# Optimization experiments

Hardware: AMD Instinct MI355X
Metric: run time of the kernel (lower is better)

Reference implementation:

```python
import jax, jax.numpy as jnp
import numpy as np

B, N, NPOINT, NSAMPLE = 8, 8192, 2048, 32
RADIUS = 0.4
C_IN = 64
MLP = [64, 64, 128]
EPS = 1e-5
BIG = 1e10


def setup_inputs() -> dict:
    key = jax.random.key(0)
    ks = jax.random.split(key, 2 + 4 * len(MLP))
    inp = {
        'xyz': jax.random.normal(ks[0], (B, N, 3), jnp.float32),
        'features': jax.random.normal(ks[1], (B, C_IN, N), jnp.float32),
    }
    last_c = C_IN + 3
    j = 2
    for i, out_c in enumerate(MLP):
        inp[f'w{i}'] = jax.random.normal(ks[j], (out_c, last_c), jnp.float32) * (1.0 / np.sqrt(last_c)); j += 1
        inp[f'b{i}'] = jax.random.normal(ks[j], (out_c,), jnp.float32) * 0.01; j += 1
        inp[f'g{i}'] = 1.0 + 0.01 * jax.random.normal(ks[j], (out_c,), jnp.float32); j += 1
        inp[f'bt{i}'] = 0.01 * jax.random.normal(ks[j], (out_c,), jnp.float32); j += 1
        last_c = out_c
    return inp


def fps(xyz, m):
    # Farthest point sampling; deterministic start at index 0 (torch uses randint).
    b, n, _ = xyz.shape

    def step(carry, _):
        dist, far = carry
        centroid = jnp.take_along_axis(xyz, far[:, None, None], axis=1)  # [B,1,3]
        d = jnp.sum((xyz - centroid) ** 2, axis=-1)                      # [B,N]
        dist = jnp.minimum(dist, d)
        new_far = jnp.argmax(dist, axis=1)
        return (dist, new_far), far

    init = (jnp.full((b, n), BIG, xyz.dtype), jnp.zeros((b,), jnp.int32))
    _, idxs = jax.lax.scan(step, init, None, length=m)
    return jnp.transpose(idxs)  # [B,m]


def ball_query(xyz, centroids, radius, k):
    # Euclidean cdist via the (a-b)^2 = a^2 + b^2 - 2ab expansion.
    x2 = jnp.sum(xyz * xyz, axis=-1)            # [B,N]
    c2 = jnp.sum(centroids * centroids, axis=-1)  # [B,M]
    d2 = c2[:, :, None] + x2[:, None, :] - 2.0 * jnp.einsum('bmd,bnd->bmn', centroids, xyz)
    d = jnp.sqrt(jnp.maximum(d2, 0.0))           # [B,M,N]
    dm = jnp.where(d <= radius, d, BIG)
    _, idx = jax.lax.top_k(-dm, k)               # k smallest distances
    return idx                                   # [B,M,K]


def gather_points(x, idx):
    # x: [B,N,C], idx: [B,M,K] -> [B,M,K,C]
    b = x.shape[0]
    return x[jnp.arange(b)[:, None, None], idx]


def reference(xyz, features, w0, b0, g0, bt0, w1, b1, g1, bt1, w2, b2, g2, bt2):
    idx = fps(xyz, NPOINT)                                   # [B,M]
    new_xyz = jnp.take_along_axis(xyz, idx[:, :, None], axis=1)  # [B,M,3]
    knn_idx = ball_query(xyz, new_xyz, RADIUS, NSAMPLE)      # [B,M,K]
    grouped_xyz = gather_points(xyz, knn_idx)                # [B,M,K,3]
    grouped_xyz_norm = grouped_xyz - new_xyz[:, :, None, :]
    grouped_feat = gather_points(jnp.transpose(features, (0, 2, 1)), knn_idx)  # [B,M,K,C]
    feat = jnp.concatenate([grouped_xyz_norm, grouped_feat], axis=-1)          # [B,M,K,C+3]

    for w, b, g, bt in ((w0, b0, g0, bt0), (w1, b1, g1, bt1), (w2, b2, g2, bt2)):
        feat = jnp.einsum('bmkc,oc->bmko', feat, w) + b      # 1x1 conv
        mu = jnp.mean(feat, axis=(0, 1, 2))                  # BN, training-mode batch stats
        var = jnp.mean((feat - mu) ** 2, axis=(0, 1, 2))
        feat = (feat - mu) * jax.lax.rsqrt(var + EPS) * g + bt
        feat = jax.nn.relu(feat)

    new_feat = jnp.max(feat, axis=2)                         # max over neighbors -> [B,M,C_out]
    return new_xyz, jnp.transpose(new_feat, (0, 2, 1))       # [B,M,3], [B,C_out,M]
```

## Files before the change

kernel.cpp:

```cpp
#include <hip/hip_runtime.h>
#include <hip/hip_bf16.h>
#include <stdint.h>

typedef unsigned short u16;
typedef unsigned int   u32;
typedef unsigned long long u64;
typedef float v2f __attribute__((ext_vector_type(2)));
typedef __attribute__((ext_vector_type(8))) short bf16x8;
typedef __attribute__((ext_vector_type(4))) float f32x4;

#define B_    8
#define N_    8192
#define M_    2048
#define NS_   32
#define CIN_  64
#define ROWS_ (B_*M_*NS_)
#define BIGF  1e10f
#define EPSF  1e-5f
#define INV_ROWS (1.0f/524288.0f)

__device__ __forceinline__ u16 f2bf(float f){
  u32 x=__float_as_uint(f);
  return (u16)((x + 0x7FFFu + ((x>>16)&1u))>>16);
}
__device__ __forceinline__ float bf2f(u16 u){ return __uint_as_float(((u32)u)<<16); }

__device__ __forceinline__ u64 wave_max_key(u64 k){
#define DPP_LVL(CTRL) { \
    u32 lo_=(u32)__builtin_amdgcn_update_dpp(0,(int)(u32)k,(CTRL),0xF,0xF,true); \
    u32 hi_=(u32)__builtin_amdgcn_update_dpp(0,(int)(u32)(k>>32),(CTRL),0xF,0xF,true); \
    u64 o_=((u64)hi_<<32)|(u64)lo_; \
    k=(o_>k)?o_:k; }
  DPP_LVL(0x111)
  DPP_LVL(0x112)
  DPP_LVL(0x114)
  DPP_LVL(0x118)
  DPP_LVL(0x142)
  DPP_LVL(0x143)
#undef DPP_LVL
  return k;
}

__global__ __launch_bounds__(256) void k_prep(
    const float* w0,const float* b0,const float* g0,const float* bt0,
    const float* w1,const float* b1,const float* g1,const float* bt1,
    const float* w2,const float* b2,const float* g2,const float* bt2,
    float* biasf,float* gf,float* btf,float* stats,
    u16* Wb0h, u16* Wb0l, u16* Wb1h, u16* Wb1l, u16* Wb2h, u16* Wb2l)
{
  int tid=threadIdx.x;
  for (int i=tid;i<768;i+=256) stats[i]=0.f;
  for (int i=tid;i<6144;i+=256){
    int e=i&7, lane=(i>>3)&63, idx=i>>9;
    int tn=idx/3, k0=idx%3;
    int col = tn*16 + (lane&15);
    int k   = k0*32 + ((lane>>4)&3)*8 + e;
    float v = 0.f;
    if (k < 64)            v = w0[col*67 + 3 + k];
    else if (k < 67)       v = w0[col*67 + (k-64)];
    u16 hib = f2bf(v);
    Wb0h[i] = hib;
    Wb0l[i] = f2bf(v - bf2f(hib));
  }
  for (int i=tid;i<4096;i+=256){
    int e=i&7, lane=(i>>3)&63, k0=(i>>9)&1, tn=i>>10;
    int col = tn*16 + (lane&15);
    int k   = k0*32 + ((lane>>4)&3)*8 + e;
    float v = w1[col*64 + k];
    u16 hib = f2bf(v);
    Wb1h[i] = hib;
    Wb1l[i] = f2bf(v - bf2f(hib));
  }
  for (int i=tid;i<8192;i+=256){
    int e=i&7, lane=(i>>3)&63, k0=(i>>9)&1, tn=i>>10;
    int col = tn*16 + (lane&15);
    int k   = k0*32 + ((lane>>4)&3)*8 + e;
    float v = w2[col*64 + k];
    u16 hib = f2bf(v);
    Wb2h[i] = hib;
    Wb2l[i] = f2bf(v - bf2f(hib));
  }
  if (tid<64){
    biasf[0*128+tid]=b0[tid]; gf[0*128+tid]=g0[tid]; btf[0*128+tid]=bt0[tid];
    biasf[1*128+tid]=b1[tid]; gf[1*128+tid]=g1[tid]; btf[1*128+tid]=bt1[tid];
  }
  if (tid<128){
    biasf[2*128+tid]=b2[tid]; gf[2*128+tid]=g2[tid]; btf[2*128+tid]=bt2[tid];
  }
}

__global__ __launch_bounds__(512) void k_fpstr(const float* __restrict__ xyz,
                                               float* __restrict__ nxyz, float* __restrict__ out0,
                                               const float* __restrict__ feats, u16* __restrict__ featT)
{
#pragma clang fp contract(off)
  __shared__ float sx[N_], sy[N_], sz[N_];
  __shared__ int sidx[M_];
  __shared__ u64 skey[2][8];
  int tid=threadIdx.x;
  if (blockIdx.x >= 8){
    float (*t)[65] = (float(*)[65])sx;
    int idx = blockIdx.x - 8;
    int bb = idx >> 7, n0 = (idx & 127) * 64;
    int a=tid&63, q=tid>>6;
    const float* fp = feats + (size_t)bb*CIN_*N_;
    #pragma unroll
    for (int s=0;s<8;s++){ int c=q*8+s; t[c][a]=fp[(size_t)c*N_ + n0 + a]; }
    __syncthreads();
    u16* op = featT + (size_t)bb*N_*CIN_;
    #pragma unroll
    for (int s=0;s<8;s++){ int n=q*8+s; op[(size_t)(n0+n)*CIN_ + a] = f2bf(t[a][n]); }
    return;
  }
  int b=blockIdx.x;
  const float* xp = xyz + (size_t)b*N_*3;
  for (int i=tid;i<N_;i+=512){ sx[i]=xp[i*3]; sy[i]=xp[i*3+1]; sz[i]=xp[i*3+2]; }
  __syncthreads();
  v2f px[8],py[8],pz[8],md[8];
  int base = tid*16;
  #pragma unroll
  for (int p=0;p<8;p++){
    px[p]=*(const v2f*)&sx[base+2*p];
    py[p]=*(const v2f*)&sy[base+2*p];
    pz[p]=*(const v2f*)&sz[base+2*p];
    v2f m0; m0[0]=BIGF; m0[1]=BIGF; md[p]=m0;
  }
  u32 invb = 0xFFFFFFFFu - (u32)base;
  int far=0;
  int lane=tid&63, wv=tid>>6;
  for (int step=0; step<M_; step++){
    if (tid==0) sidx[step]=far;
    float cxs=sx[far], cys=sy[far], czs=sz[far];
    v2f cx; cx[0]=cxs; cx[1]=cxs;
    v2f cy; cy[0]=cys; cy[1]=cys;
    v2f cz; cz[0]=czs; cz[1]=czs;
    u64 kb=0;
    #pragma unroll
    for (int p=0;p<8;p++){
      v2f dx=px[p]-cx, dy=py[p]-cy, dz=pz[p]-cz;
      v2f d=(dx*dx+dy*dy)+dz*dz;
      v2f m=__builtin_elementwise_min(md[p],d);
      md[p]=m;
      u64 k0=((u64)__float_as_uint(m[0])<<32)|(u64)(invb-(u32)(2*p));
      u64 k1=((u64)__float_as_uint(m[1])<<32)|(u64)(invb-(u32)(2*p+1));
      u64 kp=(k1>k0)?k1:k0;
      kb=(kp>kb)?kp:kb;
    }
    kb = wave_max_key(kb);
    int par = step & 1;
    if (lane==63) skey[par][wv]=kb;
    __syncthreads();
    u64 a0=skey[par][0],a1=skey[par][1],a2=skey[par][2],a3=skey[par][3];
    u64 a4=skey[par][4],a5=skey[par][5],a6=skey[par][6],a7=skey[par][7];
    a0=(a1>a0)?a1:a0; a2=(a3>a2)?a3:a2; a4=(a5>a4)?a5:a4; a6=(a7>a6)?a7:a6;
    a0=(a2>a0)?a2:a0; a4=(a6>a4)?a6:a4;
    a0=(a4>a0)?a4:a0;
    far = (int)(0xFFFFFFFFu - (u32)(a0 & 0xFFFFFFFFull));
  }
  for (int i=tid;i<M_;i+=512){
    int id = sidx[i];
    float x=sx[id], y=sy[id], z=sz[id];
    size_t o=(size_t)(b*M_+i)*3;
    nxyz[o]=x; nxyz[o+1]=y; nxyz[o+2]=z;
    out0[o]=x; out0[o+1]=y; out0[o+2]=z;
  }
}

#define BQCAP 512
__global__ __launch_bounds__(512) void k_bq(const float* __restrict__ xyz, const float* __restrict__ nxyz,
                                            int* __restrict__ knn)
{
  __shared__ float candd[8][BQCAP];
  __shared__ u16  candi[8][BQCAP];
  int tid=threadIdx.x;
  int cid0 = blockIdx.x*8;
  int b = cid0 >> 11;
  const float* xp = xyz + (size_t)b*N_*3;
  int w=tid>>6, lane=tid&63;
  int cid = cid0 + w;
  float cx=nxyz[(size_t)cid*3], cy=nxyz[(size_t)cid*3+1], cz=nxyz[(size_t)cid*3+2];
  float c2 = __fmul_rn(cx,cx);
  c2 = __fadd_rn(c2, __fmul_rn(cy,cy));
  c2 = __fadd_rn(c2, __fmul_rn(cz,cz));
  int cnt=0;
  for (int i0=0;i0<N_;i0+=64){
    int i=i0+lane;
    float x=xp[i*3], y=xp[i*3+1], z=xp[i*3+2];
    float pw = __fmul_rn(x,x);
    pw = __fadd_rn(pw, __fmul_rn(y,y));
    pw = __fadd_rn(pw, __fmul_rn(z,z));
    float dot = __fmul_rn(cx,x);
    dot = __fadd_rn(dot, __fmul_rn(cy,y));
    dot = __fadd_rn(dot, __fmul_rn(cz,z));
    float d2 = __fsub_rn(__fadd_rn(c2,pw), __fmul_rn(2.0f,dot));
    float d = sqrtf(fmaxf(d2,0.f));
    bool in = (d <= 0.4f);
    u64 msk = __ballot(in);
    int pos = cnt + __popcll(msk & ((1ull<<lane)-1ull));
    if (in && pos<BQCAP){ candd[w][pos]=d; candi[w][pos]=(u16)i; }
    cnt += __popcll(msk);
  }
  int R = cnt<BQCAP ? cnt : BQCAP;
  int* kout = knn + (size_t)cid*NS_;
  if (R >= NS_){
    for (int s=0;s<NS_;s++){
      u64 kb = ~0ull;
      for (int j=lane;j<R;j+=64){
        float v=candd[w][j];
        u64 k = ((u64)__float_as_uint(v)<<32) | (u64)(u32)j;
        kb = (k<kb)?k:kb;
      }
      u64 inv = wave_max_key(~kb);
      if (lane==63){
        u64 kw = ~inv;
        int bpp = (int)(u32)(kw & 0xFFFFFFFFull);
        kout[s]=candi[w][bpp];
        candd[w][bpp]=3e38f;
      }
    }
  } else {
    if (lane<R) kout[lane]=candi[w][lane];
    int need = NS_-R, slot = R;
    for (int i0=0; i0<N_ && need>0; i0+=64){
      int i=i0+lane;
      float x=xp[i*3], y=xp[i*3+1], z=xp[i*3+2];
      float pw = __fmul_rn(x,x);
      pw = __fadd_rn(pw, __fmul_rn(y,y));
      pw = __fadd_rn(pw, __fmul_rn(z,z));
      float dot = __fmul_rn(cx,x);
      dot = __fadd_rn(dot, __fmul_rn(cy,y));
      dot = __fadd_rn(dot, __fmul_rn(cz,z));
      float d2 = __fsub_rn(__fadd_rn(c2,pw), __fmul_rn(2.0f,dot));
      float d = sqrtf(fmaxf(d2,0.f));
      bool in = (d <= 0.4f);
      u64 mm = __ballot(!in);
      while (mm && need>0){
        int bpos = __ffsll((long long)mm)-1;
        if (lane==0) kout[slot] = i0+bpos;
        slot++; need--;
        mm &= mm-1;
      }
    }
  }
}

__global__ __launch_bounds__(256) void k_mm0(const float* __restrict__ xyz, const u16* __restrict__ featT,
                                             const int* __restrict__ knn, const float* __restrict__ nxyz,
                                             const u16* __restrict__ Wb0h, const u16* __restrict__ Wb0l,
                                             const float* __restrict__ bias0, u16* __restrict__ Y0,
                                             float* __restrict__ stats0)
{
  __shared__ u16 Xs[64*128];
  __shared__ u16 WH[12*64*8];
  __shared__ u16 WL[12*64*8];
  __shared__ float cs[128];
  int tid=threadIdx.x;
  {
    const uint4* s4=(const uint4*)Wb0h; uint4* d4=(uint4*)WH;
    const uint4* s5=(const uint4*)Wb0l; uint4* d5=(uint4*)WL;
    for (int i=tid;i<768;i+=256){ d4[i]=s4[i]; d5[i]=s5[i]; }
  }
  for (int i=tid;i<128;i+=256) cs[i]=0.f;
  int w=tid>>6, lane=tid&63;
  int rl=tid>>2, t=tid&3;
  float sSum[4]={0.f,0.f,0.f,0.f}, sSq[4]={0.f,0.f,0.f,0.f};
  __syncthreads();
  for (int tile=blockIdx.x; tile<8192; tile+=gridDim.x){
    size_t base=(size_t)tile*64;
    {
      int row=(int)base+rl;
      int bm = row>>5, b = row>>16;
      int n  = knn[row];
      const uint4* fp = (const uint4*)(featT + ((size_t)b*N_ + n)*CIN_);
      char* xr = (char*)Xs + rl*256;
      u32 swz = (u32)((rl&7)<<4);
      uint4 v0=fp[t*2], v1=fp[t*2+1];
      *(uint4*)(xr + ((t*32)    ^ swz)) = v0;
      *(uint4*)(xr + ((t*32+16) ^ swz)) = v1;
      uint4 pz = make_uint4(0u,0u,0u,0u);
      if (t==0){
        const float* cp = nxyz + (size_t)bm*3;
        const float* xp = xyz + ((size_t)b*N_ + n)*3;
        u32 w01 = (u32)f2bf(xp[0]-cp[0]) | ((u32)f2bf(xp[1]-cp[1])<<16);
        u32 w2  = (u32)f2bf(xp[2]-cp[2]);
        pz.x = w01; pz.y = w2;
      }
      *(uint4*)(xr + ((128+t*16) ^ swz)) = pz;
    }
    __syncthreads();
    f32x4 acc[4];
    #pragma unroll
    for (int tn=0;tn<4;tn++){ acc[tn][0]=0.f; acc[tn][1]=0.f; acc[tn][2]=0.f; acc[tn][3]=0.f; }
    int arow = w*16 + (lane&15);
    u32 aswz = (u32)((arow&7)<<4);
    #pragma unroll
    for (int k0=0;k0<3;k0++){
      int aoff = arow*256 + (int)(((u32)((k0*32 + ((lane>>4)&3)*8)*2)) ^ aswz);
      bf16x8 a = *(const bf16x8*)((const char*)Xs + aoff);
      #pragma unroll
      for (int tn=0;tn<4;tn++){
        bf16x8 bl = *(const bf16x8*)&WL[((tn*3+k0)*64+lane)*8];
        bf16x8 bh = *(const bf16x8*)&WH[((tn*3+k0)*64+lane)*8];
        acc[tn] = __builtin_amdgcn_mfma_f32_16x16x32_bf16(a, bl, acc[tn], 0,0,0);
        acc[tn] = __builtin_amdgcn_mfma_f32_16x16x32_bf16(a, bh, acc[tn], 0,0,0);
      }
    }
    #pragma unroll
    for (int tn=0;tn<4;tn++){
      int col = tn*16 + (lane&15);
      float bb = bias0[col];
      #pragma unroll
      for (int j=0;j<4;j++){
        int row = w*16 + (lane>>4)*4 + j;
        u16 yb = f2bf(acc[tn][j] + bb);
        Y0[(base+row)*64 + col] = yb;
        float yv = bf2f(yb);
        sSum[tn]+=yv; sSq[tn]+=yv*yv;
      }
    }
    __syncthreads();
  }
  #pragma unroll
  for (int tn=0;tn<4;tn++){
    int col = tn*16 + (lane&15);
    atomicAdd(&cs[col],    sSum[tn]);
    atomicAdd(&cs[64+col], sSq[tn]);
  }
  __syncthreads();
  if (tid<64){
    atomicAdd(&stats0[tid*2],   cs[tid]);
    atomicAdd(&stats0[tid*2+1], cs[64+tid]);
  }
}

__global__ __launch_bounds__(256) void k_mm1(u16* __restrict__ Y,
                                             const u16* __restrict__ Wb1h, const u16* __restrict__ Wb1l,
                                             const float* __restrict__ bias1, const float* __restrict__ gf0,
                                             const float* __restrict__ btf0, const float* __restrict__ stats0,
                                             float* __restrict__ stats1)
{
  __shared__ u16 Xs[64*64];
  __shared__ u16 WH[8*64*8];
  __shared__ u16 WL[8*64*8];
  __shared__ float sc[64], sh[64];
  __shared__ float cs[128];
  int tid=threadIdx.x;
  if (tid<64){
    float mu = stats0[tid*2]*INV_ROWS;
    float var= stats0[tid*2+1]*INV_ROWS - mu*mu;
    float rs = 1.0f/sqrtf(var+EPSF);
    float s  = rs*gf0[tid];
    sc[tid]=s; sh[tid]=btf0[tid]-mu*s;
  }
  {
    const uint4* sh4=(const uint4*)Wb1h; uint4* dh4=(uint4*)WH;
    const uint4* sl4=(const uint4*)Wb1l; uint4* dl4=(uint4*)WL;
    dh4[tid]=sh4[tid]; dh4[tid+256]=sh4[tid+256];
    dl4[tid]=sl4[tid]; dl4[tid+256]=sl4[tid+256];
  }
  for (int i=tid;i<128;i+=256) cs[i]=0.f;
  int w=tid>>6, lane=tid&63;
  float sSum[4]={0.f,0.f,0.f,0.f}, sSq[4]={0.f,0.f,0.f,0.f};
  __syncthreads();
  for (int tile=blockIdx.x; tile<8192; tile+=gridDim.x){
    size_t base=(size_t)tile*64;
    for (int i=tid;i<512;i+=256){
      int rl=i>>3, c0=(i&7)*8;
      uint4 v=*(const uint4*)(Y + (base+rl)*64 + c0);
      u32 arr[4]={v.x,v.y,v.z,v.w};
      u32 pk[4];
      #pragma unroll
      for (int q=0;q<4;q++){
        int cc=c0+q*2;
        float lo=bf2f((u16)(arr[q]&0xFFFFu));
        float hi=bf2f((u16)(arr[q]>>16));
        lo=fmaxf(0.f, lo*sc[cc]+sh[cc]);
        hi=fmaxf(0.f, hi*sc[cc+1]+sh[cc+1]);
        pk[q] = (u32)f2bf(lo) | ((u32)f2bf(hi)<<16);
      }
      uint4 o4; o4.x=pk[0]; o4.y=pk[1]; o4.z=pk[2]; o4.w=pk[3];
      int byteoff = rl*128 + ((c0*2) ^ ((rl&7)<<4));
      *(uint4*)((char*)Xs + byteoff) = o4;
    }
    __syncthreads();
    f32x4 acc[4];
    #pragma unroll
    for (int tn=0;tn<4;tn++){ acc[tn][0]=0.f; acc[tn][1]=0.f; acc[tn][2]=0.f; acc[tn][3]=0.f; }
    int arow = w*16 + (lane&15);
    #pragma unroll
    for (int k0=0;k0<2;k0++){
      int aoff = arow*128 + ((k0*64 + (lane>>4)*16) ^ ((arow&7)<<4));
      bf16x8 a = *(const bf16x8*)((const char*)Xs + aoff);
      #pragma unroll
      for (int tn=0;tn<4;tn++){
        bf16x8 bl = *(const bf16x8*)&WL[((tn*2+k0)*64+lane)*8];
        bf16x8 bh = *(const bf16x8*)&WH[((tn*2+k0)*64+lane)*8];
        acc[tn] = __builtin_amdgcn_mfma_f32_16x16x32_bf16(a, bl, acc[tn], 0,0,0);
        acc[tn] = __builtin_amdgcn_mfma_f32_16x16x32_bf16(a, bh, acc[tn], 0,0,0);
      }
    }
    #pragma unroll
    for (int tn=0;tn<4;tn++){
      int col = tn*16 + (lane&15);
      float bb = bias1[col];
      #pragma unroll
      for (int j=0;j<4;j++){
        int row = w*16 + (lane>>4)*4 + j;
        u16 yb = f2bf(acc[tn][j] + bb);
        Y[(base+row)*64 + col] = yb;
        float yv = bf2f(yb);
        sSum[tn]+=yv; sSq[tn]+=yv*yv;
      }
    }
    __syncthreads();
  }
  #pragma unroll
  for (int tn=0;tn<4;tn++){
    int col = tn*16 + (lane&15);
    atomicAdd(&cs[col],    sSum[tn]);
    atomicAdd(&cs[64+col], sSq[tn]);
  }
  __syncthreads();
  if (tid<64){
    atomicAdd(&stats1[tid*2],   cs[tid]);
    atomicAdd(&stats1[tid*2+1], cs[64+tid]);
  }
}

__global__ __launch_bounds__(256) void k_mm2a(const u16* __restrict__ Y1,
                                              const u16* __restrict__ Wb2h, const u16* __restrict__ Wb2l,
                                              const float* __restrict__ bias2, const float* __restrict__ gf1,
                                              const float* __restrict__ btf1, const float* __restrict__ stats1,
                                              float* __restrict__ stats2, float* __restrict__ out1)
{
  __shared__ u16 Xs[64*64];
  __shared__ u16 WH[8192];
  __shared__ u16 WL[8192];
  __shared__ float Ys[64*128];
  __shared__ float sc[64], sh[64];
  __shared__ float sred[512];
  int tid=threadIdx.x;
  if (tid<64){
    float mu = stats1[tid*2]*INV_ROWS;
    float var= stats1[tid*2+1]*INV_ROWS - mu*mu;
    float rs = 1.0f/sqrtf(var+EPSF);
    float s  = rs*gf1[tid];
    sc[tid]=s; sh[tid]=btf1[tid]-mu*s;
  }
  {
    const uint4* s4=(const uint4*)Wb2h; uint4* d4=(uint4*)WH;
    const uint4* s5=(const uint4*)Wb2l; uint4* d5=(uint4*)WL;
    for (int i=tid;i<1024;i+=256){ d4[i]=s4[i]; d5[i]=s5[i]; }
  }
  int w=tid>>6, lane=tid&63;
  int pg=tid>>7, po=tid&127;
  float accSum=0.f, accSq=0.f;
  __syncthreads();
  for (int tile=blockIdx.x; tile<8192; tile+=gridDim.x){
    size_t base=(size_t)tile*64;
    for (int i=tid;i<512;i+=256){
      int rl=i>>3, c0=(i&7)*8;
      uint4 v=*(const uint4*)(Y1 + (base+rl)*64 + c0);
      u32 arr[4]={v.x,v.y,v.z,v.w};
      u32 pk[4];
      #pragma unroll
      for (int q=0;q<4;q++){
        int cc=c0+q*2;
        float lo=bf2f((u16)(arr[q]&0xFFFFu));
        float hi=bf2f((u16)(arr[q]>>16));
        lo=fmaxf(0.f, lo*sc[cc]+sh[cc]);
        hi=fmaxf(0.f, hi*sc[cc+1]+sh[cc+1]);
        pk[q] = (u32)f2bf(lo) | ((u32)f2bf(hi)<<16);
      }
      uint4 o4; o4.x=pk[0]; o4.y=pk[1]; o4.z=pk[2]; o4.w=pk[3];
      int byteoff = rl*128 + ((c0*2) ^ ((rl&7)<<4));
      *(uint4*)((char*)Xs + byteoff) = o4;
    }
    __syncthreads();
    f32x4 acc[8];
    #pragma unroll
    for (int tn=0;tn<8;tn++){ acc[tn][0]=0.f; acc[tn][1]=0.f; acc[tn][2]=0.f; acc[tn][3]=0.f; }
    int arow = w*16 + (lane&15);
    #pragma unroll
    for (int k0=0;k0<2;k0++){
      int aoff = arow*128 + ((k0*64 + (lane>>4)*16) ^ ((arow&7)<<4));
      bf16x8 a = *(const bf16x8*)((const char*)Xs + aoff);
      #pragma unroll
      for (int tn=0;tn<8;tn++){
        bf16x8 bl = *(const bf16x8*)&WL[((tn*2+k0)*64+lane)*8];
        bf16x8 bh = *(const bf16x8*)&WH[((tn*2+k0)*64+lane)*8];
        acc[tn] = __builtin_amdgcn_mfma_f32_16x16x32_bf16(a, bl, acc[tn], 0,0,0);
        acc[tn] = __builtin_amdgcn_mfma_f32_16x16x32_bf16(a, bh, acc[tn], 0,0,0);
      }
    }
    #pragma unroll
    for (int tn=0;tn<8;tn++){
      int col = tn*16 + (lane&15);
      float bb = bias2[col];
      #pragma unroll
      for (int j=0;j<4;j++){
        int row = w*16 + (lane>>4)*4 + j;
        int byteoff = row*512 + ((col*4) ^ ((row&7)<<4));
        *(float*)((char*)Ys + byteoff) = acc[tn][j] + bb;
      }
    }
    __syncthreads();
    {
      float mx=-3e38f;
      #pragma unroll 4
      for (int k=0;k<32;k++){
        int row = pg*32 + k;
        int byteoff = row*512 + ((po*4) ^ ((row&7)<<4));
        float y = *(const float*)((const char*)Ys + byteoff);
        accSum += y; accSq += y*y;
        mx = fmaxf(mx, y);
      }
      int bm = tile*2 + pg; int bi = bm>>11, m = bm&2047;
      out1[((size_t)bi*128+po)*M_ + m] = mx;
    }
    __syncthreads();
  }
  sred[tid]      = accSum;
  sred[256+tid]  = accSq;
  __syncthreads();
  if (tid<128){
    float s = sred[tid] + sred[tid+128];
    float q = sred[256+tid] + sred[256+tid+128];
    atomicAdd(&stats2[tid*2],   s);
    atomicAdd(&stats2[tid*2+1], q);
  }
}

__global__ __launch_bounds__(256) void k_pool(float* __restrict__ out1, const float* __restrict__ stats2,
                                              const float* __restrict__ gf2, const float* __restrict__ btf2)
{
  int idx = blockIdx.x*256 + threadIdx.x;
  int o = (idx >> 11) & 127;
  float mu = stats2[o*2]*INV_ROWS;
  float var= stats2[o*2+1]*INV_ROWS - mu*mu;
  float rs = 1.0f/sqrtf(var+EPSF);
  float s  = rs*gf2[o];
  float sh = btf2[o]-mu*s;
  out1[idx] = fmaxf(0.f, out1[idx]*s + sh);
}

extern "C" void kernel_launch(void* const* d_in, const int* in_sizes, int n_in,
                              void* d_out, int out_size, void* d_ws, size_t ws_size,
                              hipStream_t stream)
{
  (void)in_sizes; (void)n_in; (void)out_size; (void)ws_size;
  const float* xyz =(const float*)d_in[0];
  const float* feat=(const float*)d_in[1];
  const float* w0=(const float*)d_in[2],  *b0=(const float*)d_in[3],  *g0=(const float*)d_in[4],  *bt0=(const float*)d_in[5];
  const float* w1=(const float*)d_in[6],  *b1=(const float*)d_in[7],  *g1=(const float*)d_in[8],  *bt1=(const float*)d_in[9];
  const float* w2=(const float*)d_in[10], *b2=(const float*)d_in[11], *g2=(const float*)d_in[12], *bt2=(const float*)d_in[13];
  float* out0=(float*)d_out;
  float* out1=out0 + (size_t)B_*M_*3;

  char* ws=(char*)d_ws;
  float* nxyz =(float*)(ws);
  u16*   Wb1h =(u16*)  (ws + 196608);
  u16*   Wb1l =(u16*)  (ws + 204800);
  u16*   Wb2h =(u16*)  (ws + 212992);
  u16*   Wb2l =(u16*)  (ws + 229376);
  int*   knn  =(int*)  (ws + 262144);
  u16*   Wb0h =(u16*)  (ws + 2359296);
  u16*   Wb0l =(u16*)  (ws + 2376704);
  float* biasf=(float*)(ws + 2425856);
  float* gfp  =(float*)(ws + 2427392);
  float* btfp =(float*)(ws + 2428928);
  float* stats=(float*)(ws + 2430464);
  u16*   featT=(u16*)  (ws + 2433536);
  u16*   Y0   =(u16*)  (ws + 10822144);

  k_prep<<<1,256,0,stream>>>(w0,b0,g0,bt0,w1,b1,g1,bt1,w2,b2,g2,bt2,biasf,gfp,btfp,stats,
                             Wb0h,Wb0l,Wb1h,Wb1l,Wb2h,Wb2l);
  k_fpstr<<<8+1024,512,0,stream>>>(xyz, nxyz, out0, feat, featT);
  k_bq<<<2048,512,0,stream>>>(xyz, nxyz, knn);
  k_mm0<<<512,256,0,stream>>>(xyz, featT, knn, nxyz, Wb0h, Wb0l, biasf+0, Y0, stats+0);
  k_mm1<<<512,256,0,stream>>>(Y0, Wb1h, Wb1l, biasf+128, gfp+0, btfp+0, stats+0, stats+256);
  k_mm2a<<<512,256,0,stream>>>(Y0, Wb2h, Wb2l, biasf+256, gfp+128, btfp+128, stats+256, stats+512, out1);
  k_pool<<<8192,256,0,stream>>>(out1, stats+512, gfp+256, btfp+256);
}
```

Before: 2.186 ms.

## Fuse prep into FPS kernel, radix-select ball query top-k, vectorize pool

```diff
diff --git a/kernel.cpp b/kernel.cpp
--- a/kernel.cpp
+++ b/kernel.cpp
@@ -41,63 +41,61 @@
   return k;
 }
 
-__global__ __launch_bounds__(256) void k_prep(
+__global__ __launch_bounds__(512) void k_fpstr(const float* __restrict__ xyz,
+                                               float* __restrict__ nxyz, float* __restrict__ out0,
+                                               const float* __restrict__ feats, u16* __restrict__ featT,
     const float* w0,const float* b0,const float* g0,const float* bt0,
     const float* w1,const float* b1,const float* g1,const float* bt1,
     const float* w2,const float* b2,const float* g2,const float* bt2,
     float* biasf,float* gf,float* btf,float* stats,
     u16* Wb0h, u16* Wb0l, u16* Wb1h, u16* Wb1l, u16* Wb2h, u16* Wb2l)
 {
-  int tid=threadIdx.x;
-  for (int i=tid;i<768;i+=256) stats[i]=0.f;
-  for (int i=tid;i<6144;i+=256){
-    int e=i&7, lane=(i>>3)&63, idx=i>>9;
-    int tn=idx/3, k0=idx%3;
-    int col = tn*16 + (lane&15);
-    int k   = k0*32 + ((lane>>4)&3)*8 + e;
-    float v = 0.f;
-    if (k < 64)            v = w0[col*67 + 3 + k];
-    else if (k < 67)       v = w0[col*67 + (k-64)];
-    u16 hib = f2bf(v);
-    Wb0h[i] = hib;
-    Wb0l[i] = f2bf(v - bf2f(hib));
-  }
-  for (int i=tid;i<4096;i+=256){
-    int e=i&7, lane=(i>>3)&63, k0=(i>>9)&1, tn=i>>10;
-    int col = tn*16 + (lane&15);
-    int k   = k0*32 + ((lane>>4)&3)*8 + e;
-    float v = w1[col*64 + k];
-    u16 hib = f2bf(v);
-    Wb1h[i] = hib;
-    Wb1l[i] = f2bf(v - bf2f(hib));
-  }
-  for (int i=tid;i<8192;i+=256){
-    int e=i&7, lane=(i>>3)&63, k0=(i>>9)&1, tn=i>>10;
-    int col = tn*16 + (lane&15);
-    int k   = k0*32 + ((lane>>4)&3)*8 + e;
-    float v = w2[col*64 + k];
-    u16 hib = f2bf(v);
-    Wb2h[i] = hib;
-    Wb2l[i] = f2bf(v - bf2f(hib));
-  }
-  if (tid<64){
-    biasf[0*128+tid]=b0[tid]; gf[0*128+tid]=g0[tid]; btf[0*128+tid]=bt0[tid];
-    biasf[1*128+tid]=b1[tid]; gf[1*128+tid]=g1[tid]; btf[1*128+tid]=bt1[tid];
-  }
-  if (tid<128){
-    biasf[2*128+tid]=b2[tid]; gf[2*128+tid]=g2[tid]; btf[2*128+tid]=bt2[tid];
-  }
-}
-
-__global__ __launch_bounds__(512) void k_fpstr(const float* __restrict__ xyz,
-                                               float* __restrict__ nxyz, float* __restrict__ out0,
-                                               const float* __restrict__ feats, u16* __restrict__ featT)
-{
 #pragma clang fp contract(off)
   __shared__ float sx[N_], sy[N_], sz[N_];
   __shared__ int sidx[M_];
   __shared__ u64 skey[2][8];
   int tid=threadIdx.x;
+  if (blockIdx.x >= 1032){
+    for (int i=tid;i<768;i+=512) stats[i]=0.f;
+    for (int i=tid;i<6144;i+=512){
+      int e=i&7, lane=(i>>3)&63, idx=i>>9;
+      int tn=idx/3, k0=idx%3;
+      int col = tn*16 + (lane&15);
+      int k   = k0*32 + ((lane>>4)&3)*8 + e;
+      float v = 0.f;
+      if (k < 64)            v = w0[col*67 + 3 + k];
+      else if (k < 67)       v = w0[col*67 + (k-64)];
+      u16 hib = f2bf(v);
+      Wb0h[i] = hib;
+      Wb0l[i] = f2bf(v - bf2f(hib));
+    }
+    for (int i=tid;i<4096;i+=512){
+      int e=i&7, lane=(i>>3)&63, k0=(i>>9)&1, tn=i>>10;
+      int col = tn*16 + (lane&15);
+      int k   = k0*32 + ((lane>>4)&3)*8 + e;
+      float v = w1[col*64 + k];
+      u16 hib = f2bf(v);
+      Wb1h[i] = hib;
+      Wb1l[i] = f2bf(v - bf2f(hib));
+    }
+    for (int i=tid;i<8192;i+=512){
+      int e=i&7, lane=(i>>3)&63, k0=(i>>9)&1, tn=i>>10;
+      int col = tn*16 + (lane&15);
+      int k   = k0*32 + ((lane>>4)&3)*8 + e;
+      float v = w2[col*64 + k];
+      u16 hib = f2bf(v);
+      Wb2h[i] = hib;
+      Wb2l[i] = f2bf(v - bf2f(hib));
+    }
+    if (tid<64){
+      biasf[0*128+tid]=b0[tid]; gf[0*128+tid]=g0[tid]; btf[0*128+tid]=bt0[tid];
+      biasf[1*128+tid]=b1[tid]; gf[1*128+tid]=g1[tid]; btf[1*128+tid]=bt1[tid];
+    }
+    if (tid<128){
+      biasf[2*128+tid]=b2[tid]; gf[2*128+tid]=g2[tid]; btf[2*128+tid]=bt2[tid];
+    }
+    return;
+  }
   if (blockIdx.x >= 8){
     float (*t)[65] = (float(*)[65])sx;
     int idx = blockIdx.x - 8;
@@ -203,20 +201,40 @@
   int R = cnt<BQCAP ? cnt : BQCAP;
   int* kout = knn + (size_t)cid*NS_;
   if (R >= NS_){
-    for (int s=0;s<NS_;s++){
-      u64 kb = ~0ull;
-      for (int j=lane;j<R;j+=64){
-        float v=candd[w][j];
-        u64 k = ((u64)__float_as_uint(v)<<32) | (u64)(u32)j;
-        kb = (k<kb)?k:kb;
-      }
-      u64 inv = wave_max_key(~kb);
-      if (lane==63){
-        u64 kw = ~inv;
-        int bpp = (int)(u32)(kw & 0xFFFFFFFFull);
-        kout[s]=candi[w][bpp];
-        candd[w][bpp]=3e38f;
-      }
+    u32 cb[8];
+    #pragma unroll
+    for (int q=0;q<8;q++){
+      int j=lane+q*64;
+      cb[q] = (j<R) ? __float_as_uint(candd[w][j]) : 0x7F7FFFFFu;
+    }
+    u32 lo=0u, hi=0x3F000000u;
+    while (lo < hi){
+      u32 mid=(lo+hi)>>1;
+      int c=0;
+      #pragma unroll
+      for (int q=0;q<8;q++) c += (int)__popcll(__ballot(cb[q]<=mid));
+      if (c >= NS_) hi=mid; else lo=mid+1;
+    }
+    u32 theta=hi;
+    int outPos=0;
+    #pragma unroll
+    for (int q=0;q<8;q++){
+      int j=lane+q*64;
+      bool v = (cb[q] < theta);
+      u64 mk=__ballot(v);
+      int pos = outPos + (int)__popcll(mk & ((1ull<<lane)-1ull));
+      if (v) kout[pos]=candi[w][j];
+      outPos += (int)__popcll(mk);
+    }
+    #pragma unroll
+    for (int q=0;q<8;q++){
+      if (outPos >= NS_) break;
+      int j=lane+q*64;
+      bool v = (cb[q] == theta);
+      u64 mk=__ballot(v);
+      int pos = outPos + (int)__popcll(mk & ((1ull<<lane)-1ull));
+      if (v && pos<NS_) kout[pos]=candi[w][j];
+      outPos += (int)__popcll(mk);
     }
   } else {
     if (lane<R) kout[lane]=candi[w][lane];
@@ -534,14 +552,19 @@
 __global__ __launch_bounds__(256) void k_pool(float* __restrict__ out1, const float* __restrict__ stats2,
                                               const float* __restrict__ gf2, const float* __restrict__ btf2)
 {
-  int idx = blockIdx.x*256 + threadIdx.x;
-  int o = (idx >> 11) & 127;
+  int idx4 = blockIdx.x*256 + threadIdx.x;
+  int o = (idx4 >> 9) & 127;
   float mu = stats2[o*2]*INV_ROWS;
   float var= stats2[o*2+1]*INV_ROWS - mu*mu;
   float rs = 1.0f/sqrtf(var+EPSF);
   float s  = rs*gf2[o];
   float sh = btf2[o]-mu*s;
-  out1[idx] = fmaxf(0.f, out1[idx]*s + sh);
+  float4 v = ((const float4*)out1)[idx4];
+  v.x=fmaxf(0.f, v.x*s+sh);
+  v.y=fmaxf(0.f, v.y*s+sh);
+  v.z=fmaxf(0.f, v.z*s+sh);
+  v.w=fmaxf(0.f, v.w*s+sh);
+  ((float4*)out1)[idx4]=v;
 }
 
 extern "C" void kernel_launch(void* const* d_in, const int* in_sizes, int n_in,
@@ -573,12 +596,13 @@
   u16*   featT=(u16*)  (ws + 2433536);
   u16*   Y0   =(u16*)  (ws + 10822144);
 
-  k_prep<<<1,256,0,stream>>>(w0,b0,g0,bt0,w1,b1,g1,bt1,w2,b2,g2,bt2,biasf,gfp,btfp,stats,
-                             Wb0h,Wb0l,Wb1h,Wb1l,Wb2h,Wb2l);
-  k_fpstr<<<8+1024,512,0,stream>>>(xyz, nxyz, out0, feat, featT);
+  k_fpstr<<<8+1024+1,512,0,stream>>>(xyz, nxyz, out0, feat, featT,
+                                     w0,b0,g0,bt0,w1,b1,g1,bt1,w2,b2,g2,bt2,
+                                     biasf,gfp,btfp,stats,
+                                     Wb0h,Wb0l,Wb1h,Wb1l,Wb2h,Wb2l);
   k_bq<<<2048,512,0,stream>>>(xyz, nxyz, knn);
   k_mm0<<<512,256,0,stream>>>(xyz, featT, knn, nxyz, Wb0h, Wb0l, biasf+0, Y0, stats+0);
   k_mm1<<<512,256,0,stream>>>(Y0, Wb1h, Wb1l, biasf+128, gfp+0, btfp+0, stats+0, stats+256);
   k_mm2a<<<512,256,0,stream>>>(Y0, Wb2h, Wb2l, biasf+256, gfp+128, btfp+128, stats+256, stats+512, out1);
-  k_pool<<<8192,256,0,stream>>>(out1, stats+512, gfp+256, btfp+256);
-}
+  k_pool<<<2048,256,0,stream>>>(out1, stats+512, gfp+256, btfp+256);
+}
```

Result: no change. 2.172 ms (-0.6%).
